# Kernel optimization log

Measured on AMD Instinct MI355X. Metric: run time of the kernel, lower is better.

Reference implementation:

```python
import jax, jax.numpy as jnp
import numpy as np

B, FIN, FOUT, N_TASKS = 256, 1024, 512, 20
FOUT2 = 2 * FOUT  # ConditionalLinear is built with 2*fout


def setup_inputs() -> dict:
    key = jax.random.key(0)
    k1, k2, k3 = jax.random.split(key, 3)
    x = jax.random.normal(k1, (B, FIN), dtype=jnp.float32)
    task_id = jax.random.randint(k2, (B,), 0, N_TASKS)
    # Embedding table [n_tasks, fin*2*fout]; kaiming_normal(fan_out) std = sqrt(2/fout2)
    std = np.sqrt(2.0 / FOUT2).astype(np.float32)
    W = jax.random.normal(k3, (N_TASKS, FIN * FOUT2), dtype=jnp.float32) * std
    return {"x": x, "task_id": task_id, "W": W}


def reference(x, task_id, W):
    Bsz, fin = x.shape
    fout2 = W.shape[1] // fin
    # task-conditional weight gather: [B, 2*fout, fin]
    w = W[task_id].reshape(Bsz, fout2, fin)
    # per-sample matvec (torch.bmm with x.unsqueeze(2))
    logits = jnp.einsum('boi,bi->bo', w, x).reshape(Bsz, fout2 // 2, 2)
    # BinaryGumbelSoftmax eval path: h = 1 - argmax(softmax(logits)) = 1 - argmax(logits)
    h = 1.0 - jnp.argmax(logits, axis=-1).astype(logits.dtype)
    return (h, logits)
```

## Files before the change

### kernel.cpp

```cpp
#include <hip/hip_runtime.h>

#define FIN   1024
#define FOUT2 1024
#define NTASK 20
#define BSZ   256
#define HOFF  (256 * 512)

__global__ __launch_bounds__(256, 2)
void cond_linear_kernel(const float* __restrict__ x,
                        const int* __restrict__ task_id,
                        const float* __restrict__ W,
                        float* __restrict__ out) {
    __shared__ int sh_ord[BSZ];
    __shared__ int wcnt[4];
    __shared__ int sh_n;

    const int tid  = threadIdx.x;
    const int lane = tid & 63;
    const int wv   = tid >> 6;
    const int bx   = blockIdx.x;
    const int t    = bx >> 7;
    const int rem  = bx & 127;
    const int tile = rem & 63;
    const int slot = rem >> 6;
    const int o0   = tile * 16 + wv * 4;

    const int my_task = task_id[tid];
    const bool match = (my_task == t);
    const unsigned long long m64 = __ballot(match);
    if (lane == 0) wcnt[wv] = __popcll(m64);
    __syncthreads();
    int base = 0;
    #pragma unroll
    for (int w = 0; w < 4; ++w)
        if (w < wv) base += wcnt[w];
    if (match) {
        const int pos = base + __popcll(m64 & ((1ull << lane) - 1ull));
        sh_ord[pos] = tid;
    }
    if (tid == 0) sh_n = wcnt[0] + wcnt[1] + wcnt[2] + wcnt[3];
    __syncthreads();
    const int n = sh_n;
    const int half = (n + 1) >> 1;
    const int i0 = slot ? half : 0;
    const int i1 = slot ? n    : half;
    if (i0 >= i1) return;

    const float* Wt = W + (size_t)t * (FOUT2 * FIN);
    float4 wr[4][4];
    #pragma unroll
    for (int r = 0; r < 4; ++r) {
        const float4* wp = (const float4*)(Wt + (size_t)(o0 + r) * FIN);
        #pragma unroll
        for (int p = 0; p < 4; ++p)
            wr[r][p] = wp[p * 64 + lane];
    }
    #pragma unroll
    for (int r = 0; r < 4; ++r)
        #pragma unroll
        for (int p = 0; p < 4; ++p)
            asm volatile("" : "+v"(wr[r][p].x), "+v"(wr[r][p].y),
                              "+v"(wr[r][p].z), "+v"(wr[r][p].w));

    const bool hi32 = (lane & 32) != 0;
    const bool hi16 = (lane & 16) != 0;
    const bool hi8  = (lane & 8)  != 0;

    int sa = sh_ord[i0];
    int sb = sh_ord[(i0 + 1 < i1) ? i0 + 1 : i1 - 1];
    float4 xa[4], xb[4];
    #pragma unroll
    for (int p = 0; p < 4; ++p)
        xa[p] = ((const float4*)(x + (size_t)sa * FIN))[p * 64 + lane];
    #pragma unroll
    for (int p = 0; p < 4; ++p)
        xb[p] = ((const float4*)(x + (size_t)sb * FIN))[p * 64 + lane];

    for (int i = i0; i < i1; i += 2) {
        const int ina = (i + 2 < i1) ? i + 2 : i1 - 1;
        const int inb = (i + 3 < i1) ? i + 3 : i1 - 1;
        const int na_s = sh_ord[ina];
        const int nb_s = sh_ord[inb];
        float4 na[4], nb[4];
        #pragma unroll
        for (int p = 0; p < 4; ++p)
            na[p] = ((const float4*)(x + (size_t)na_s * FIN))[p * 64 + lane];
        #pragma unroll
        for (int p = 0; p < 4; ++p)
            nb[p] = ((const float4*)(x + (size_t)nb_s * FIN))[p * 64 + lane];

        float a0 = 0.f, a1 = 0.f, a2 = 0.f, a3 = 0.f;
        float b0 = 0.f, b1 = 0.f, b2 = 0.f, b3 = 0.f;
        #pragma unroll
        for (int p = 0; p < 4; ++p) {
            const float4 u = xa[p];
            const float4 v = xb[p];
            a0 += wr[0][p].x * u.x + wr[0][p].y * u.y + wr[0][p].z * u.z + wr[0][p].w * u.w;
            a1 += wr[1][p].x * u.x + wr[1][p].y * u.y + wr[1][p].z * u.z + wr[1][p].w * u.w;
            a2 += wr[2][p].x * u.x + wr[2][p].y * u.y + wr[2][p].z * u.z + wr[2][p].w * u.w;
            a3 += wr[3][p].x * u.x + wr[3][p].y * u.y + wr[3][p].z * u.z + wr[3][p].w * u.w;
            b0 += wr[0][p].x * v.x + wr[0][p].y * v.y + wr[0][p].z * v.z + wr[0][p].w * v.w;
            b1 += wr[1][p].x * v.x + wr[1][p].y * v.y + wr[1][p].z * v.z + wr[1][p].w * v.w;
            b2 += wr[2][p].x * v.x + wr[2][p].y * v.y + wr[2][p].z * v.z + wr[2][p].w * v.w;
            b3 += wr[3][p].x * v.x + wr[3][p].y * v.y + wr[3][p].z * v.z + wr[3][p].w * v.w;
        }

        const float t0 = a0 + __shfl_xor(a0, 32, 64);
        const float t1 = a1 + __shfl_xor(a1, 32, 64);
        const float t2 = a2 + __shfl_xor(a2, 32, 64);
        const float t3 = a3 + __shfl_xor(a3, 32, 64);
        const float t4 = b0 + __shfl_xor(b0, 32, 64);
        const float t5 = b1 + __shfl_xor(b1, 32, 64);
        const float t6 = b2 + __shfl_xor(b2, 32, 64);
        const float t7 = b3 + __shfl_xor(b3, 32, 64);
        float w0 = hi32 ? t4 : t0;
        float w1 = hi32 ? t5 : t1;
        float w2 = hi32 ? t6 : t2;
        float w3 = hi32 ? t7 : t3;
        w0 += __shfl_xor(w0, 16, 64);
        w1 += __shfl_xor(w1, 16, 64);
        w2 += __shfl_xor(w2, 16, 64);
        w3 += __shfl_xor(w3, 16, 64);
        float u0 = hi16 ? w2 : w0;
        float u1 = hi16 ? w3 : w1;
        u0 += __shfl_xor(u0, 8, 64);
        u1 += __shfl_xor(u1, 8, 64);
        float z = hi8 ? u1 : u0;
        z += __shfl_xor(z, 4, 64);
        z += __shfl_xor(z, 2, 64);
        z += __shfl_xor(z, 1, 64);
        const float zp = __shfl_xor(z, 8, 64);

        const int r_id = (hi8 ? 1 : 0) + (hi16 ? 2 : 0);
        const int s_idx = hi32 ? sb : sa;
        if ((lane & 7) == 0) {
            out[HOFF + (size_t)s_idx * FOUT2 + o0 + r_id] = z;
            if (!hi8) {
                out[(size_t)s_idx * (FOUT2 / 2) + (o0 >> 1) + (hi16 ? 1 : 0)]
                    = (z >= zp) ? 1.0f : 0.0f;
            }
        }

        sa = na_s; sb = nb_s;
        #pragma unroll
        for (int p = 0; p < 4; ++p) { xa[p] = na[p]; xb[p] = nb[p]; }
    }
}

extern "C" void kernel_launch(void* const* d_in, const int* in_sizes, int n_in,
                              void* d_out, int out_size, void* d_ws, size_t ws_size,
                              hipStream_t stream) {
    const float* x       = (const float*)d_in[0];
    const int*   task_id = (const int*)d_in[1];
    const float* W       = (const float*)d_in[2];
    float*       out     = (float*)d_out;

    dim3 grid(NTASK * 64 * 2);
    dim3 block(BSZ);
    hipLaunchKernelGGL(cond_linear_kernel, grid, block, 0, stream,
                       x, task_id, W, out);
}
```

Measured before the change: 31.60 us.

## Use single-wave blocks with ballot-based task compaction and XCD-aware block swizzle

```diff
diff --git a/kernel.cpp b/kernel.cpp
--- a/kernel.cpp
+++ b/kernel.cpp
@@ -3,48 +3,26 @@
 #define FIN   1024
 #define FOUT2 1024
 #define NTASK 20
-#define BSZ   256
+#define NRG   256
+#define NSLOT 2
+#define NW    (NTASK * NRG * NSLOT)
 #define HOFF  (256 * 512)
 
-__global__ __launch_bounds__(256, 2)
+__global__ __launch_bounds__(64, 2)
 void cond_linear_kernel(const float* __restrict__ x,
                         const int* __restrict__ task_id,
                         const float* __restrict__ W,
                         float* __restrict__ out) {
-    __shared__ int sh_ord[BSZ];
-    __shared__ int wcnt[4];
-    __shared__ int sh_n;
+    __shared__ int sh_ord[64];
 
-    const int tid  = threadIdx.x;
-    const int lane = tid & 63;
-    const int wv   = tid >> 6;
-    const int bx   = blockIdx.x;
-    const int t    = bx >> 7;
-    const int rem  = bx & 127;
-    const int tile = rem & 63;
-    const int slot = rem >> 6;
-    const int o0   = tile * 16 + wv * 4;
-
-    const int my_task = task_id[tid];
-    const bool match = (my_task == t);
-    const unsigned long long m64 = __ballot(match);
-    if (lane == 0) wcnt[wv] = __popcll(m64);
-    __syncthreads();
-    int base = 0;
-    #pragma unroll
-    for (int w = 0; w < 4; ++w)
-        if (w < wv) base += wcnt[w];
-    if (match) {
-        const int pos = base + __popcll(m64 & ((1ull << lane) - 1ull));
-        sh_ord[pos] = tid;
-    }
-    if (tid == 0) sh_n = wcnt[0] + wcnt[1] + wcnt[2] + wcnt[3];
-    __syncthreads();
-    const int n = sh_n;
-    const int half = (n + 1) >> 1;
-    const int i0 = slot ? half : 0;
-    const int i1 = slot ? n    : half;
-    if (i0 >= i1) return;
+    const int lane = threadIdx.x;
+    const int bid  = blockIdx.x;
+    const int orig = (bid & 7) * (NW / 8) + (bid >> 3);
+    const int t    = orig >> 9;
+    const int r2   = orig & 511;
+    const int rg   = r2 >> 1;
+    const int slot = r2 & 1;
+    const int o0   = rg * 4;
 
     const float* Wt = W + (size_t)t * (FOUT2 * FIN);
     float4 wr[4][4];
@@ -55,6 +33,29 @@
         for (int p = 0; p < 4; ++p)
             wr[r][p] = wp[p * 64 + lane];
     }
+
+    const int4 ids = ((const int4*)task_id)[lane];
+    const unsigned long long m0 = __ballot(ids.x == t);
+    const unsigned long long m1 = __ballot(ids.y == t);
+    const unsigned long long m2 = __ballot(ids.z == t);
+    const unsigned long long m3 = __ballot(ids.w == t);
+    const unsigned long long below = (1ull << lane) - 1ull;
+    int rank = __popcll(m0 & below) + __popcll(m1 & below)
+             + __popcll(m2 & below) + __popcll(m3 & below);
+    if (ids.x == t) sh_ord[rank] = 4 * lane + 0;
+    rank += (int)((m0 >> lane) & 1);
+    if (ids.y == t) sh_ord[rank] = 4 * lane + 1;
+    rank += (int)((m1 >> lane) & 1);
+    if (ids.z == t) sh_ord[rank] = 4 * lane + 2;
+    rank += (int)((m2 >> lane) & 1);
+    if (ids.w == t) sh_ord[rank] = 4 * lane + 3;
+
+    const int n = __popcll(m0) + __popcll(m1) + __popcll(m2) + __popcll(m3);
+    const int half = (n + 1) >> 1;
+    const int i0 = slot ? half : 0;
+    const int i1 = slot ? n    : half;
+    if (i0 >= i1) return;
+
     #pragma unroll
     for (int r = 0; r < 4; ++r)
         #pragma unroll
@@ -155,8 +156,8 @@
     const float* W       = (const float*)d_in[2];
     float*       out     = (float*)d_out;
 
-    dim3 grid(NTASK * 64 * 2);
-    dim3 block(BSZ);
+    dim3 grid(NW);
+    dim3 block(64);
     hipLaunchKernelGGL(cond_linear_kernel, grid, block, 0, stream,
                        x, task_id, W, out);
 }
```

Result: faster. 29.44 us (-6.8%).
